# Kernel optimization log

Hardware: AMD Instinct MI355X
Metric: run time of the kernel (lower is better)

## Reference

```python
import jax, jax.numpy as jnp
import numpy as np

MD = 4            # max displacement (pad of 8 total => 4 per side)
WIN = 2 * MD + 1  # 9x9 window -> 81 displacement channels


def setup_inputs() -> dict:
    key = jax.random.key(0)
    k1, k2 = jax.random.split(key)
    B, C, H, W = 8, 256, 128, 128
    inp = jax.random.normal(k1, (B, WIN * WIN, H, W), dtype=jnp.float32)
    second = jax.random.normal(k2, (B, C, H, W), dtype=jnp.float32)
    return {"input": inp, "second": second}


def reference(input, second):
    # out[b,c,y,x] = (1/C) * sum_{p,o in [-MD,MD]} input[b,(p+MD)*9+(o+MD),y,x]
    #                * second[b,c,y+p,x+o]  (zero padding outside)
    B, C, H, W = second.shape
    pad = jnp.pad(second, ((0, 0), (0, 0), (MD, MD), (MD, MD)))
    out = jnp.zeros((B, C, H, W), dtype=second.dtype)
    for p in range(-MD, MD + 1):          # fixed 9x9 window, not a data dim
        for o in range(-MD, MD + 1):
            d = (p + MD) * WIN + (o + MD)
            shifted = pad[:, :, p + MD:p + MD + H, o + MD:o + MD + W]  # [B,C,H,W]
            out = out + input[:, d, None, :, :] * shifted
    return out / jnp.asarray(C, dtype=second.dtype)
```

## Files before the change

kernel.cpp:

```cpp
#include <hip/hip_runtime.h>


#define MD 4
#define WIN 9

constexpr int Bc = 8, Cc = 256, Hc = 128, Wc = 128;
constexpr int TH = 16, TW = 16;
constexpr int NSLOT = 8;
constexpr int NC = 4;
constexpr int CHUNK = NSLOT * NC;
constexpr int NCHUNK = Cc / CHUNK;
constexpr int SROWS = TH + 2 * MD;
constexpr int SCOLS = TW + 2 * MD;
constexpr int CH_STRIDE = SROWS * SCOLS + 4;
constexpr int NPIX = 8;

__global__ __launch_bounds__(256, 2)
void fct_kernel(const float* __restrict__ inp,
                const float* __restrict__ second,
                float* __restrict__ out)
{
    __shared__ float sS[CHUNK * CH_STRIDE];

    const int tid   = threadIdx.x;
    const int slot  = tid & (NSLOT - 1);
    const int group = tid >> 3;
    const int r     = group >> 1;
    const int seg   = group & 1;

    const int bx   = blockIdx.x;
    const int b    = bx >> 6;
    const int tile = bx & 63;
    const int th0  = (tile >> 3) * TH;
    const int tw0  = (tile & 7) * TW;

    const int h   = th0 + r;
    const int wc0 = tw0 + seg * NPIX;

    {
        float4 z = make_float4(0.f, 0.f, 0.f, 0.f);
        float4* s4 = reinterpret_cast<float4*>(sS);
        for (int i = tid; i < CHUNK * CH_STRIDE / 4; i += 256) s4[i] = z;
    }

    const float* wbase = inp + ((size_t)b * 81 * Hc + (size_t)h) * Wc + wc0;

    const float scale = 1.0f / (float)Cc;

    for (int chunk = 0; chunk < NCHUNK; ++chunk) {
        __syncthreads();

        {
            const int c0 = chunk * CHUNK;
            #pragma unroll 1
            for (int it = 0; it < 18; ++it) {
                int q     = it * 256 + tid;
                int t     = q % 6;
                int rowch = q / 6;
                int row   = rowch % SROWS;
                int ch    = rowch / SROWS;
                int grow  = th0 - MD + row;
                int gcol  = tw0 - MD + 4 * t;
                if (grow >= 0 && grow < Hc && gcol >= 0 && gcol <= Wc - 4) {
                    const float4 v = *reinterpret_cast<const float4*>(
                        second + (((size_t)(b * Cc + c0 + ch)) * Hc + grow) * Wc + gcol);
                    *reinterpret_cast<float4*>(&sS[ch * CH_STRIDE + row * SCOLS + 4 * t]) = v;
                }
            }
        }
        __syncthreads();

        float acc[NC][NPIX];
        #pragma unroll
        for (int j = 0; j < NC; ++j)
            #pragma unroll
            for (int i = 0; i < NPIX; ++i) acc[j][i] = 0.f;

        #pragma unroll 1
        for (int P = 0; P < 9; ++P) {
            float wv[9][8];
            #pragma unroll
            for (int o = 0; o < 9; ++o) {
                const float* wp = wbase + (size_t)(P * 9 + o) * (Hc * Wc);
                float4 a0 = *reinterpret_cast<const float4*>(wp);
                float4 a1 = *reinterpret_cast<const float4*>(wp + 4);
                wv[o][0] = a0.x; wv[o][1] = a0.y; wv[o][2] = a0.z; wv[o][3] = a0.w;
                wv[o][4] = a1.x; wv[o][5] = a1.y; wv[o][6] = a1.z; wv[o][7] = a1.w;
            }
            #pragma unroll
            for (int j = 0; j < NC; ++j) {
                const int cl = j * NSLOT + slot;
                const float* srow = &sS[cl * CH_STRIDE + (r + P) * SCOLS + seg * NPIX];
                float s[16];
                #pragma unroll
                for (int t = 0; t < 4; ++t) {
                    float4 v = *reinterpret_cast<const float4*>(srow + 4 * t);
                    s[4 * t] = v.x; s[4 * t + 1] = v.y; s[4 * t + 2] = v.z; s[4 * t + 3] = v.w;
                }
                #pragma unroll
                for (int o = 0; o < 9; ++o)
                    #pragma unroll
                    for (int i = 0; i < NPIX; ++i)
                        acc[j][i] = fmaf(wv[o][i], s[i + o], acc[j][i]);
            }
        }

        #pragma unroll
        for (int j = 0; j < NC; ++j) {
            const int c = chunk * CHUNK + j * NSLOT + slot;
            float* op = out + (((size_t)(b * Cc + c)) * Hc + h) * Wc + wc0;
            float4 v0 = make_float4(acc[j][0] * scale, acc[j][1] * scale,
                                    acc[j][2] * scale, acc[j][3] * scale);
            float4 v1 = make_float4(acc[j][4] * scale, acc[j][5] * scale,
                                    acc[j][6] * scale, acc[j][7] * scale);
            *reinterpret_cast<float4*>(op)     = v0;
            *reinterpret_cast<float4*>(op + 4) = v1;
        }
    }
}

extern "C" void kernel_launch(void* const* d_in, const int* in_sizes, int n_in,
                              void* d_out, int out_size, void* d_ws, size_t ws_size,
                              hipStream_t stream) {
    const float* inp    = (const float*)d_in[0];
    const float* second = (const float*)d_in[1];
    float* outp         = (float*)d_out;

    dim3 grid(Bc * (Hc / TH) * (Wc / TW));
    dim3 block(256);
    fct_kernel<<<grid, block, 0, stream>>>(inp, second, outp);
}
```

Baseline: 439.7 us.

## Stage second tile via direct global-to-LDS loads and double-buffer weight loads

Replaces the register round-trip staging of the second-tensor tile with __builtin_amdgcn_global_load_lds direct copies using a flat slot layout, and fully unrolls that loop. Weight rows for the next displacement row are loaded into a second register buffer while the current one is consumed, overlapping global latency with FMAs. Output stores become nontemporal. The double weight buffer raises register pressure (36 float4), and the direct-to-LDS addressing relies on each wave writing a contiguous 64-slot block, which must match the per-channel stride layout.

```diff
diff --git a/kernel.cpp b/kernel.cpp
--- a/kernel.cpp
+++ b/kernel.cpp
@@ -2,9 +2,9 @@
 
 
 #define MD 4
-#define WIN 9
 
 constexpr int Bc = 8, Cc = 256, Hc = 128, Wc = 128;
+constexpr int HW = Hc * Wc;
 constexpr int TH = 16, TW = 16;
 constexpr int NSLOT = 8;
 constexpr int NC = 4;
@@ -13,7 +13,47 @@
 constexpr int SROWS = TH + 2 * MD;
 constexpr int SCOLS = TW + 2 * MD;
 constexpr int CH_STRIDE = SROWS * SCOLS + 4;
+constexpr int SLOTS_PER_CH = CH_STRIDE / 4;
+constexpr int TOT_SLOTS = CHUNK * SLOTS_PER_CH;
 constexpr int NPIX = 8;
+
+typedef float f32x4 __attribute__((ext_vector_type(4)));
+
+#define LOADW(dst, PP)                                                  \
+    {                                                                   \
+        _Pragma("unroll")                                               \
+        for (int o = 0; o < 9; ++o) {                                   \
+            const float* wp = wbase + (size_t)((PP) * 9 + o) * HW;      \
+            dst[2 * o]     = *reinterpret_cast<const float4*>(wp);      \
+            dst[2 * o + 1] = *reinterpret_cast<const float4*>(wp + 4);  \
+        }                                                               \
+    }
+
+#define COMPUTE(wcur, PP)                                                        \
+    {                                                                            \
+        _Pragma("unroll")                                                        \
+        for (int j = 0; j < NC; ++j) {                                           \
+            const int cl = j * NSLOT + slot;                                     \
+            const float* srow = &sS[cl * CH_STRIDE + (r + (PP)) * SCOLS + seg * NPIX]; \
+            float s[16];                                                         \
+            _Pragma("unroll")                                                    \
+            for (int t = 0; t < 4; ++t) {                                        \
+                float4 v = *reinterpret_cast<const float4*>(srow + 4 * t);       \
+                s[4*t] = v.x; s[4*t+1] = v.y; s[4*t+2] = v.z; s[4*t+3] = v.w;    \
+            }                                                                    \
+            _Pragma("unroll")                                                    \
+            for (int o = 0; o < 9; ++o) {                                        \
+                acc[j][0] = fmaf(wcur[2*o].x,   s[o + 0], acc[j][0]);            \
+                acc[j][1] = fmaf(wcur[2*o].y,   s[o + 1], acc[j][1]);            \
+                acc[j][2] = fmaf(wcur[2*o].z,   s[o + 2], acc[j][2]);            \
+                acc[j][3] = fmaf(wcur[2*o].w,   s[o + 3], acc[j][3]);            \
+                acc[j][4] = fmaf(wcur[2*o+1].x, s[o + 4], acc[j][4]);            \
+                acc[j][5] = fmaf(wcur[2*o+1].y, s[o + 5], acc[j][5]);            \
+                acc[j][6] = fmaf(wcur[2*o+1].z, s[o + 6], acc[j][6]);            \
+                acc[j][7] = fmaf(wcur[2*o+1].w, s[o + 7], acc[j][7]);            \
+            }                                                                    \
+        }                                                                        \
+    }
 
 __global__ __launch_bounds__(256, 2)
 void fct_kernel(const float* __restrict__ inp,
@@ -27,6 +67,7 @@
     const int group = tid >> 3;
     const int r     = group >> 1;
     const int seg   = group & 1;
+    const int wid   = tid >> 6;
 
     const int bx   = blockIdx.x;
     const int b    = bx >> 6;
@@ -40,31 +81,40 @@
     {
         float4 z = make_float4(0.f, 0.f, 0.f, 0.f);
         float4* s4 = reinterpret_cast<float4*>(sS);
-        for (int i = tid; i < CHUNK * CH_STRIDE / 4; i += 256) s4[i] = z;
+        for (int i = tid; i < TOT_SLOTS; i += 256) s4[i] = z;
     }
 
-    const float* wbase = inp + ((size_t)b * 81 * Hc + (size_t)h) * Wc + wc0;
-
+    const float* wbase = inp + (size_t)b * 81 * HW + (size_t)h * Wc + wc0;
     const float scale = 1.0f / (float)Cc;
 
     for (int chunk = 0; chunk < NCHUNK; ++chunk) {
         __syncthreads();
 
+        float4 wA[18], wB[18];
+
+        LOADW(wA, 0);
+
         {
             const int c0 = chunk * CHUNK;
-            #pragma unroll 1
-            for (int it = 0; it < 18; ++it) {
-                int q     = it * 256 + tid;
-                int t     = q % 6;
-                int rowch = q / 6;
-                int row   = rowch % SROWS;
-                int ch    = rowch / SROWS;
-                int grow  = th0 - MD + row;
-                int gcol  = tw0 - MD + 4 * t;
-                if (grow >= 0 && grow < Hc && gcol >= 0 && gcol <= Wc - 4) {
-                    const float4 v = *reinterpret_cast<const float4*>(
-                        second + (((size_t)(b * Cc + c0 + ch)) * Hc + grow) * Wc + gcol);
-                    *reinterpret_cast<float4*>(&sS[ch * CH_STRIDE + row * SCOLS + 4 * t]) = v;
+            #pragma unroll
+            for (int it = 0; it < 19; ++it) {
+                const int m = it * 256 + tid;
+                if (m < TOT_SLOTS) {
+                    const int ch   = m / SLOTS_PER_CH;
+                    const int k    = m - ch * SLOTS_PER_CH;
+                    const int row  = k / 6;
+                    const int x    = k - row * 6;
+                    const int grow = th0 - MD + row;
+                    const int gcol = tw0 - MD + 4 * x;
+                    float* ldsb = &sS[(it * 256 + wid * 64) * 4];
+                    if (k < 144 && grow >= 0 && grow < Hc && gcol >= 0 && gcol <= Wc - 4) {
+                        const float* gp = second +
+                            (((size_t)(b * Cc + c0 + ch)) * Hc + grow) * Wc + gcol;
+                        __builtin_amdgcn_global_load_lds(
+                            (const __attribute__((address_space(1))) void*)gp,
+                            (__attribute__((address_space(3))) void*)ldsb,
+                            16, 0, 0);
+                    }
                 }
             }
         }
@@ -77,31 +127,12 @@
             for (int i = 0; i < NPIX; ++i) acc[j][i] = 0.f;
 
         #pragma unroll 1
-        for (int P = 0; P < 9; ++P) {
-            float wv[9][8];
-            #pragma unroll
-            for (int o = 0; o < 9; ++o) {
-                const float* wp = wbase + (size_t)(P * 9 + o) * (Hc * Wc);
-                float4 a0 = *reinterpret_cast<const float4*>(wp);
-                float4 a1 = *reinterpret_cast<const float4*>(wp + 4);
-                wv[o][0] = a0.x; wv[o][1] = a0.y; wv[o][2] = a0.z; wv[o][3] = a0.w;
-                wv[o][4] = a1.x; wv[o][5] = a1.y; wv[o][6] = a1.z; wv[o][7] = a1.w;
-            }
-            #pragma unroll
-            for (int j = 0; j < NC; ++j) {
-                const int cl = j * NSLOT + slot;
-                const float* srow = &sS[cl * CH_STRIDE + (r + P) * SCOLS + seg * NPIX];
-                float s[16];
-                #pragma unroll
-                for (int t = 0; t < 4; ++t) {
-                    float4 v = *reinterpret_cast<const float4*>(srow + 4 * t);
-                    s[4 * t] = v.x; s[4 * t + 1] = v.y; s[4 * t + 2] = v.z; s[4 * t + 3] = v.w;
-                }
-                #pragma unroll
-                for (int o = 0; o < 9; ++o)
-                    #pragma unroll
-                    for (int i = 0; i < NPIX; ++i)
-                        acc[j][i] = fmaf(wv[o][i], s[i + o], acc[j][i]);
+        for (int Ph = 0; Ph < 9; Ph += 2) {
+            if (Ph + 1 < 9) LOADW(wB, Ph + 1);
+            COMPUTE(wA, Ph);
+            if (Ph + 1 < 9) {
+                if (Ph + 2 < 9) LOADW(wA, Ph + 2);
+                COMPUTE(wB, Ph + 1);
             }
         }
 
@@ -109,12 +140,12 @@
         for (int j = 0; j < NC; ++j) {
             const int c = chunk * CHUNK + j * NSLOT + slot;
             float* op = out + (((size_t)(b * Cc + c)) * Hc + h) * Wc + wc0;
-            float4 v0 = make_float4(acc[j][0] * scale, acc[j][1] * scale,
-                                    acc[j][2] * scale, acc[j][3] * scale);
-            float4 v1 = make_float4(acc[j][4] * scale, acc[j][5] * scale,
-                                    acc[j][6] * scale, acc[j][7] * scale);
-            *reinterpret_cast<float4*>(op)     = v0;
-            *reinterpret_cast<float4*>(op + 4) = v1;
+            f32x4 v0 = { acc[j][0] * scale, acc[j][1] * scale,
+                         acc[j][2] * scale, acc[j][3] * scale };
+            f32x4 v1 = { acc[j][4] * scale, acc[j][5] * scale,
+                         acc[j][6] * scale, acc[j][7] * scale };
+            __builtin_nontemporal_store(v0, reinterpret_cast<f32x4*>(op));
+            __builtin_nontemporal_store(v1, reinterpret_cast<f32x4*>(op + 4));
         }
     }
 }
```

Result: slower. 465.5 us (+5.9%).

## Load halo tiles via global_load_lds, halve channel chunk, raise occupancy

Applied to the files above, without the earlier changes.

Loads the padded `second` tile straight into LDS with `__builtin_amdgcn_global_load_lds` instead of going through registers, using a linear slot layout so each wave writes a contiguous LDS range. Halves channels per chunk (NC 4→2) and raises launch bounds to 4 blocks per CU, trading fewer accumulators and a smaller LDS footprint for more occupancy. The cost is that the 81 weight values are reloaded twice as often per output, because there are twice as many chunks. The direct-to-LDS path relies on the hardware lane-address layout matching the slot math, and the LDS wait before the barrier is implicit.

```diff
diff --git a/kernel.cpp b/kernel.cpp
--- a/kernel.cpp
+++ b/kernel.cpp
@@ -2,31 +2,34 @@
 
 
 #define MD 4
-#define WIN 9
 
 constexpr int Bc = 8, Cc = 256, Hc = 128, Wc = 128;
+constexpr int HW = Hc * Wc;
 constexpr int TH = 16, TW = 16;
 constexpr int NSLOT = 8;
-constexpr int NC = 4;
+constexpr int NC = 2;
 constexpr int CHUNK = NSLOT * NC;
 constexpr int NCHUNK = Cc / CHUNK;
 constexpr int SROWS = TH + 2 * MD;
 constexpr int SCOLS = TW + 2 * MD;
 constexpr int CH_STRIDE = SROWS * SCOLS + 4;
+constexpr int SLOTS_PER_CH = CH_STRIDE / 4;
+constexpr int TOT_SLOTS = CHUNK * SLOTS_PER_CH;
 constexpr int NPIX = 8;
 
-__global__ __launch_bounds__(256, 2)
+__global__ __launch_bounds__(256, 4)
 void fct_kernel(const float* __restrict__ inp,
                 const float* __restrict__ second,
                 float* __restrict__ out)
 {
-    __shared__ float sS[CHUNK * CH_STRIDE];
+    __shared__ __attribute__((aligned(16))) float sS[CHUNK * CH_STRIDE];
 
     const int tid   = threadIdx.x;
     const int slot  = tid & (NSLOT - 1);
     const int group = tid >> 3;
     const int r     = group >> 1;
     const int seg   = group & 1;
+    const int wid   = tid >> 6;
 
     const int bx   = blockIdx.x;
     const int b    = bx >> 6;
@@ -40,31 +43,38 @@
     {
         float4 z = make_float4(0.f, 0.f, 0.f, 0.f);
         float4* s4 = reinterpret_cast<float4*>(sS);
-        for (int i = tid; i < CHUNK * CH_STRIDE / 4; i += 256) s4[i] = z;
+        #pragma unroll 1
+        for (int i = tid; i < TOT_SLOTS; i += 256) s4[i] = z;
     }
 
-    const float* wbase = inp + ((size_t)b * 81 * Hc + (size_t)h) * Wc + wc0;
-
+    const float* wbase = inp + (size_t)b * 81 * HW + (size_t)h * Wc + wc0;
     const float scale = 1.0f / (float)Cc;
 
+    #pragma unroll 1
     for (int chunk = 0; chunk < NCHUNK; ++chunk) {
         __syncthreads();
 
         {
             const int c0 = chunk * CHUNK;
-            #pragma unroll 1
-            for (int it = 0; it < 18; ++it) {
-                int q     = it * 256 + tid;
-                int t     = q % 6;
-                int rowch = q / 6;
-                int row   = rowch % SROWS;
-                int ch    = rowch / SROWS;
-                int grow  = th0 - MD + row;
-                int gcol  = tw0 - MD + 4 * t;
-                if (grow >= 0 && grow < Hc && gcol >= 0 && gcol <= Wc - 4) {
-                    const float4 v = *reinterpret_cast<const float4*>(
-                        second + (((size_t)(b * Cc + c0 + ch)) * Hc + grow) * Wc + gcol);
-                    *reinterpret_cast<float4*>(&sS[ch * CH_STRIDE + row * SCOLS + 4 * t]) = v;
+            #pragma unroll
+            for (int it = 0; it < 10; ++it) {
+                const int m = it * 256 + tid;
+                if (m < TOT_SLOTS) {
+                    const int ch   = m / SLOTS_PER_CH;
+                    const int k    = m - ch * SLOTS_PER_CH;
+                    const int row  = k / 6;
+                    const int x    = k - row * 6;
+                    const int grow = th0 - MD + row;
+                    const int gcol = tw0 - MD + 4 * x;
+                    float* ldsb = &sS[(size_t)(it * 256 + wid * 64) * 4];
+                    if (k < 144 && grow >= 0 && grow < Hc && gcol >= 0 && gcol <= Wc - 4) {
+                        const float* gp = second +
+                            (((size_t)(b * Cc + c0 + ch)) * Hc + grow) * Wc + gcol;
+                        __builtin_amdgcn_global_load_lds(
+                            (const __attribute__((address_space(1))) void*)gp,
+                            (__attribute__((address_space(3))) void*)ldsb,
+                            16, 0, 0);
+                    }
                 }
             }
         }
@@ -81,7 +91,7 @@
             float wv[9][8];
             #pragma unroll
             for (int o = 0; o < 9; ++o) {
-                const float* wp = wbase + (size_t)(P * 9 + o) * (Hc * Wc);
+                const float* wp = wbase + (size_t)(P * 9 + o) * HW;
                 float4 a0 = *reinterpret_cast<const float4*>(wp);
                 float4 a1 = *reinterpret_cast<const float4*>(wp + 4);
                 wv[o][0] = a0.x; wv[o][1] = a0.y; wv[o][2] = a0.z; wv[o][3] = a0.w;
@@ -95,7 +105,7 @@
                 #pragma unroll
                 for (int t = 0; t < 4; ++t) {
                     float4 v = *reinterpret_cast<const float4*>(srow + 4 * t);
-                    s[4 * t] = v.x; s[4 * t + 1] = v.y; s[4 * t + 2] = v.z; s[4 * t + 3] = v.w;
+                    s[4*t] = v.x; s[4*t+1] = v.y; s[4*t+2] = v.z; s[4*t+3] = v.w;
                 }
                 #pragma unroll
                 for (int o = 0; o < 9; ++o)
```

Result: slower. 577.7 us (+31.4%).
